# Optimization experiments

Hardware: AMD Instinct MI355X
Metric: run time of the kernel (lower is better)

The kernel has to match this reference:

```python
import jax, jax.numpy as jnp
import numpy as np

B, H, W = 4, 256, 256
DIM = 180
NH = 6
WH, WW = 16, 16          # window size
BH, BW = 8, 8            # base window size
CH = DIM // (2 * NH)     # per-head dim = 15
SCALE = float(CH)        # note: divide by head_dim (not sqrt), as in source
RH, RW = WH // BH, WW // BW
R = RH * RW              # spatial reduction ratio = 4
L = WH * WW              # 256 tokens per window
BL = BH * BW             # 64 base tokens
POS_DIM = (DIM // 4) // 4  # 11


def _rel_index(Hs, Ws):
    coords = np.stack(np.meshgrid(np.arange(Hs), np.arange(Ws), indexing='ij')).reshape(2, -1)
    rel = (coords[:, :, None] - coords[:, None, :]).transpose(1, 2, 0)
    rel[..., 0] += Hs - 1
    rel[..., 1] += Ws - 1
    rel[..., 0] *= 2 * Ws - 1
    return rel.sum(-1)  # (L, L) int

RPI = _rel_index(WH, WW)


def _ln(x, g, b):
    mu = x.mean(-1, keepdims=True)
    var = ((x - mu) ** 2).mean(-1, keepdims=True)
    return (x - mu) / jnp.sqrt(var + 1e-5) * g + b


def _conv(x, w, b):  # x: NHWC, w: HWIO
    y = jax.lax.conv_general_dilated(x, w, (1, 1), 'SAME',
                                     dimension_numbers=('NHWC', 'HWIO', 'NHWC'))
    return y + b


def setup_inputs():
    key = jax.random.key(0)
    ks = jax.random.split(key, 12)
    def wgt(k, shape, s=0.05):
        return jax.random.normal(k, shape, jnp.float32) * s
    C5 = DIM // 5
    d = {}
    d['x'] = jax.random.normal(ks[0], (B, H, W, DIM), jnp.float32)
    d['dfe_c1_w'] = wgt(ks[1], (1, 1, DIM, C5)); d['dfe_c1_b'] = jnp.zeros((C5,), jnp.float32)
    d['dfe_c2_w'] = wgt(ks[2], (3, 3, C5, C5));  d['dfe_c2_b'] = jnp.zeros((C5,), jnp.float32)
    d['dfe_c3_w'] = wgt(ks[3], (1, 1, C5, DIM)); d['dfe_c3_b'] = jnp.zeros((DIM,), jnp.float32)
    d['dfe_lin_w'] = wgt(ks[4], (1, 1, DIM, DIM)); d['dfe_lin_b'] = jnp.zeros((DIM,), jnp.float32)
    d['sl_w'] = wgt(ks[5], (1, R), 0.5); d['sl_b'] = jnp.zeros((1,), jnp.float32)
    d['pos_proj_w'] = wgt(ks[6], (POS_DIM, 2), 0.1); d['pos_proj_b'] = jnp.zeros((POS_DIM,), jnp.float32)
    for i, kk in zip((1, 2), (ks[7], ks[8])):
        d['pos%d_ln_g' % i] = jnp.ones((POS_DIM,), jnp.float32)
        d['pos%d_ln_b' % i] = jnp.zeros((POS_DIM,), jnp.float32)
        d['pos%d_w' % i] = wgt(kk, (POS_DIM, POS_DIM), 0.1)
        d['pos%d_b' % i] = jnp.zeros((POS_DIM,), jnp.float32)
    d['pos3_ln_g'] = jnp.ones((POS_DIM,), jnp.float32)
    d['pos3_ln_b'] = jnp.zeros((POS_DIM,), jnp.float32)
    d['pos3_w'] = wgt(ks[9], (NH, POS_DIM), 0.1)
    d['pos3_b'] = jnp.zeros((NH,), jnp.float32)
    d['proj_w'] = wgt(ks[10], (DIM, DIM))
    d['proj_b'] = jnp.zeros((DIM,), jnp.float32)
    return d


def reference(x, dfe_c1_w, dfe_c1_b, dfe_c2_w, dfe_c2_b, dfe_c3_w, dfe_c3_b,
              dfe_lin_w, dfe_lin_b, sl_w, sl_b, pos_proj_w, pos_proj_b,
              pos1_ln_g, pos1_ln_b, pos1_w, pos1_b,
              pos2_ln_g, pos2_ln_b, pos2_w, pos2_b,
              pos3_ln_g, pos3_ln_b, pos3_w, pos3_b,
              proj_w, proj_b):
    Bb, Hh, Ww_, C = x.shape
    # ---- DFE: qv = conv_path(x) * linear_path(x) ----
    t = jax.nn.leaky_relu(_conv(x, dfe_c1_w, dfe_c1_b), 0.2)
    t = jax.nn.leaky_relu(_conv(t, dfe_c2_w, dfe_c2_b), 0.2)
    t = _conv(t, dfe_c3_w, dfe_c3_b)
    qv = t * _conv(x, dfe_lin_w, dfe_lin_b)  # (B,H,W,C)
    # ---- window partition ----
    qv = qv.reshape(Bb, Hh // WH, WH, Ww_ // WW, WW, C).transpose(0, 1, 3, 2, 4, 5)
    qv = qv.reshape(-1, L, C)                       # (B_, L, C)
    B_ = qv.shape[0]
    qv = qv.reshape(B_, L, 2, NH, CH)
    q = qv[:, :, 0].transpose(0, 2, 1, 3)           # (B_, NH, L, CH)
    v = qv[:, :, 1].transpose(0, 2, 1, 3)           # (B_, NH, L, CH)
    # ---- spatial linear projection of v to base window ----
    vp = v.reshape(B_, NH, BH, RH, BW, RW, CH).transpose(0, 1, 2, 4, 6, 3, 5)
    vp = vp.reshape(B_, NH, BL, CH, R)
    vp = jnp.einsum('bnlcr,r->bnlc', vp, sl_w[0]) + sl_b[0]  # (B_, NH, BL, CH)
    # ---- spatial self-correlation ----
    corr = jnp.einsum('bnlc,bnmc->bnlm', q, vp) / SCALE       # (B_, NH, L, BL)
    # dynamic relative position bias (non-residual MLP)
    ph = jnp.arange(1 - WH, WH)
    pw = jnp.arange(1 - WW, WW)
    biases = jnp.stack(jnp.meshgrid(ph, pw, indexing='ij')).reshape(2, -1).T.astype(x.dtype)
    p = biases @ pos_proj_w.T + pos_proj_b
    p = jax.nn.relu(_ln(p, pos1_ln_g, pos1_ln_b)) @ pos1_w.T + pos1_b
    p = jax.nn.relu(_ln(p, pos2_ln_g, pos2_ln_b)) @ pos2_w.T + pos2_b
    pos = jax.nn.relu(_ln(p, pos3_ln_g, pos3_ln_b)) @ pos3_w.T + pos3_b  # ((2WH-1)(2WW-1), NH)
    rpb = pos[RPI.reshape(-1)].reshape(L, L, NH).transpose(2, 0, 1)      # (NH, L, L)
    rpb = rpb.reshape(NH, L, BH, RH, BW, RW).transpose(0, 1, 2, 4, 3, 5)
    rpb = rpb.reshape(NH, L, BL, R).mean(-1)                             # (NH, L, BL)
    corr = corr + rpb[None]
    x_sp = jnp.einsum('bnlm,bnmc->bnlc', corr, vp)
    x_sp = x_sp.transpose(0, 2, 1, 3).reshape(B_, L, C // 2)
    # ---- channel self-correlation (single-head) ----
    qc = q.transpose(0, 2, 1, 3).reshape(B_, L, C // 2)
    vc = v.transpose(0, 2, 1, 3).reshape(B_, L, C // 2)
    cmap = jnp.einsum('blc,bld->bcd', qc, vc) / float(L)                 # (B_, C/2, C/2)
    x_ch = jnp.einsum('bcd,bld->blc', cmap, vc)                          # (B_, L, C/2)
    # ---- window reverse + fuse ----
    def rev(a):
        c = a.shape[-1]
        a = a.reshape(Bb, Hh // WH, Ww_ // WW, WH, WW, c).transpose(0, 1, 3, 2, 4, 5)
        return a.reshape(Bb, Hh, Ww_, c)
    x_sp = rev(x_sp.reshape(B_, WH, WW, C // 2))
    x_ch = rev(x_ch.reshape(B_, WH, WW, C // 2))
    out = jnp.concatenate([x_sp, x_ch], -1) @ proj_w.T + proj_b          # (B,H,W,C)
    return out
```

## Files before the change

kernel.cpp:

```cpp
#include <hip/hip_runtime.h>

#define LEAKY(v) ((v) > 0.f ? (v) : 0.2f * (v))

__device__ __forceinline__ void ln_relu11(float* p, const float* __restrict__ g,
                                          const float* __restrict__ b) {
  float mu = 0.f;
#pragma unroll
  for (int j = 0; j < 11; ++j) mu += p[j];
  mu *= (1.f / 11.f);
  float var = 0.f;
#pragma unroll
  for (int j = 0; j < 11; ++j) { float d = p[j] - mu; var += d * d; }
  var *= (1.f / 11.f);
  float inv = 1.f / sqrtf(var + 1e-5f);
#pragma unroll
  for (int j = 0; j < 11; ++j) {
    float v = (p[j] - mu) * inv * g[j] + b[j];
    p[j] = v > 0.f ? v : 0.f;
  }
}

__global__ void pos_mlp_kernel(
    const float* __restrict__ w0, const float* __restrict__ b0,
    const float* __restrict__ g1, const float* __restrict__ be1,
    const float* __restrict__ w1, const float* __restrict__ b1,
    const float* __restrict__ g2, const float* __restrict__ be2,
    const float* __restrict__ w2, const float* __restrict__ b2,
    const float* __restrict__ g3, const float* __restrict__ be3,
    const float* __restrict__ w3, const float* __restrict__ b3,
    float* __restrict__ pos_out) {
  int r = blockIdx.x * 256 + threadIdx.x;
  if (r >= 961) return;
  float bh = (float)(r / 31 - 15);
  float bw = (float)(r % 31 - 15);
  float p[11], q[11];
#pragma unroll
  for (int j = 0; j < 11; ++j) p[j] = bh * w0[2 * j] + bw * w0[2 * j + 1] + b0[j];
  ln_relu11(p, g1, be1);
#pragma unroll
  for (int j = 0; j < 11; ++j) {
    float s = b1[j];
#pragma unroll
    for (int k = 0; k < 11; ++k) s += p[k] * w1[j * 11 + k];
    q[j] = s;
  }
  ln_relu11(q, g2, be2);
#pragma unroll
  for (int j = 0; j < 11; ++j) {
    float s = b2[j];
#pragma unroll
    for (int k = 0; k < 11; ++k) s += q[k] * w2[j * 11 + k];
    p[j] = s;
  }
  ln_relu11(p, g3, be3);
#pragma unroll
  for (int n = 0; n < 6; ++n) {
    float s = b3[n];
#pragma unroll
    for (int k = 0; k < 11; ++k) s += p[k] * w3[n * 11 + k];
    pos_out[r * 6 + n] = s;
  }
}

__global__ void rpb_kernel(const float* __restrict__ pos, float* __restrict__ rpb) {
  int o = blockIdx.x * 256 + threadIdx.x;
  int n = o >> 14;
  int l = (o >> 6) & 255;
  int m = o & 63;
  int i1 = l >> 4, j1 = l & 15;
  int bi = m >> 3, bj = m & 7;
  float s = 0.f;
#pragma unroll
  for (int rh = 0; rh < 2; ++rh)
#pragma unroll
    for (int rw = 0; rw < 2; ++rw) {
      int i2 = bi * 2 + rh, j2 = bj * 2 + rw;
      int idx = (i1 - i2 + 15) * 31 + (j1 - j2 + 15);
      s += pos[idx * 6 + n];
    }
  rpb[o] = s * 0.25f;
}

__global__ void pt_kernel(const float* __restrict__ pjw, float* __restrict__ pt) {
  int i = blockIdx.x * 256 + threadIdx.x;
  if (i >= 180 * 180) return;
  int c = i / 180, k = i % 180;
  pt[c * 180 + k] = pjw[k * 180 + c];
}

__global__ __launch_bounds__(256) void dfe1_kernel(const float* __restrict__ x,
                                                   const float* __restrict__ w1,
                                                   const float* __restrict__ b1,
                                                   float* __restrict__ t1) {
  __shared__ float xt[256][36];
  int t = threadIdx.x;
  int p0 = blockIdx.x * 256;
  float acc[36];
#pragma unroll
  for (int j = 0; j < 36; ++j) acc[j] = 0.f;
  for (int kc = 0; kc < 5; ++kc) {
    __syncthreads();
    for (int idx = t; idx < 256 * 36; idx += 256) {
      int px = idx / 36, ci = idx % 36;
      xt[px][ci] = x[(p0 + px) * 180 + kc * 36 + ci];
    }
    __syncthreads();
    for (int ci = 0; ci < 36; ++ci) {
      float v = xt[t][ci];
      const float* wr = &w1[(kc * 36 + ci) * 36];
#pragma unroll
      for (int j = 0; j < 36; ++j) acc[j] += v * wr[j];
    }
  }
  float* o = &t1[(p0 + t) * 36];
#pragma unroll
  for (int j = 0; j < 36; ++j) {
    float v = acc[j] + b1[j];
    o[j] = LEAKY(v);
  }
}

__global__ __launch_bounds__(256) void dfe2_kernel(const float* __restrict__ t1,
                                                   const float* __restrict__ w2,
                                                   const float* __restrict__ b2,
                                                   float* __restrict__ t2) {
  __shared__ float halo[18][18][36];
  int t = threadIdx.x;
  int blk = blockIdx.x;
  int img = blk >> 8;
  int rem = blk & 255;
  int ty0 = (rem >> 4) << 4;
  int tx0 = (rem & 15) << 4;
  for (int idx = t; idx < 18 * 18 * 36; idx += 256) {
    int ci = idx % 36;
    int xx = (idx / 36) % 18;
    int yy = idx / (36 * 18);
    int gy = ty0 + yy - 1;
    int gx = tx0 + xx - 1;
    float v = 0.f;
    if (gy >= 0 && gy < 256 && gx >= 0 && gx < 256)
      v = t1[((img * 256 + gy) * 256 + gx) * 36 + ci];
    halo[yy][xx][ci] = v;
  }
  __syncthreads();
  int ly = t >> 4, lx = t & 15;
  float acc[36];
#pragma unroll
  for (int j = 0; j < 36; ++j) acc[j] = 0.f;
#pragma unroll
  for (int kh = 0; kh < 3; ++kh)
#pragma unroll
    for (int kw = 0; kw < 3; ++kw) {
      for (int ci = 0; ci < 36; ++ci) {
        float v = halo[ly + kh][lx + kw][ci];
        const float* wr = &w2[((kh * 3 + kw) * 36 + ci) * 36];
#pragma unroll
        for (int j = 0; j < 36; ++j) acc[j] += v * wr[j];
      }
    }
  float* o = &t2[((img * 256 + ty0 + ly) * 256 + tx0 + lx) * 36];
#pragma unroll
  for (int j = 0; j < 36; ++j) {
    float v = acc[j] + b2[j];
    o[j] = LEAKY(v);
  }
}

__global__ __launch_bounds__(256, 2) void dfe3_kernel(const float* __restrict__ x,
                                                      const float* __restrict__ t2,
                                                      const float* __restrict__ w3,
                                                      const float* __restrict__ b3,
                                                      const float* __restrict__ wl,
                                                      const float* __restrict__ bl,
                                                      float* __restrict__ qv) {
  __shared__ __align__(16) float As[36 * 132];
  __shared__ __align__(16) float Bs[36 * 180 + 16];
  int t = threadIdx.x;
  int tx = t & 15;
  int ty = t >> 4;
  int p0 = blockIdx.x * 128;

  int pA0 = t / 9,           cA0 = t - pA0 * 9;
  int pA1 = (t + 256) / 9,   cA1 = (t + 256) - pA1 * 9;
  int pA2 = (t + 512) / 9,   cA2 = (t + 512) - pA2 * 9;
  int pA3 = (t + 768) / 9,   cA3 = (t + 768) - pA3 * 9;
  int pA4 = (t + 1024) / 9,  cA4 = (t + 1024) - pA4 * 9;
  const float4* xf4  = (const float4*)x;
  const float4* t2f4 = (const float4*)t2;
  const float4* wlf4 = (const float4*)wl;
  const float4* w3f4 = (const float4*)w3;
  float4* Bs4 = (float4*)Bs;

  float4 a0, a1, a2, a3, a4;
  float4 bF0, bF1, bF2, bF3, bF4, bF5, bF6;
  a4 = make_float4(0.f, 0.f, 0.f, 0.f);
  bF6 = make_float4(0.f, 0.f, 0.f, 0.f);

  auto scatterA = [&](int pa, int ca, float4 v) {
    As[(ca * 4 + 0) * 132 + pa] = v.x;
    As[(ca * 4 + 1) * 132 + pa] = v.y;
    As[(ca * 4 + 2) * 132 + pa] = v.z;
    As[(ca * 4 + 3) * 132 + pa] = v.w;
  };
  auto stage_write = [&]() {
    scatterA(pA0, cA0, a0);
    scatterA(pA1, cA1, a1);
    scatterA(pA2, cA2, a2);
    scatterA(pA3, cA3, a3);
    if (t < 128) scatterA(pA4, cA4, a4);
    Bs4[t] = bF0;
    Bs4[t + 256] = bF1;
    Bs4[t + 512] = bF2;
    Bs4[t + 768] = bF3;
    Bs4[t + 1024] = bF4;
    Bs4[t + 1280] = bF5;
    if (t < 84) Bs4[t + 1536] = bF6;
  };

  auto issue_lin = [&](int kc) {
    int kb = kc * 9;
    a0 = xf4[(size_t)(p0 + pA0) * 45 + kb + cA0];
    a1 = xf4[(size_t)(p0 + pA1) * 45 + kb + cA1];
    a2 = xf4[(size_t)(p0 + pA2) * 45 + kb + cA2];
    a3 = xf4[(size_t)(p0 + pA3) * 45 + kb + cA3];
    if (t < 128) a4 = xf4[(size_t)(p0 + pA4) * 45 + kb + cA4];
    int kw = kc * 1620;
    bF0 = wlf4[kw + t];
    bF1 = wlf4[kw + t + 256];
    bF2 = wlf4[kw + t + 512];
    bF3 = wlf4[kw + t + 768];
    bF4 = wlf4[kw + t + 1024];
    bF5 = wlf4[kw + t + 1280];
    if (t < 84) bF6 = wlf4[kw + t + 1536];
  };
  auto issue_conv = [&]() {
    a0 = t2f4[(size_t)(p0 + pA0) * 9 + cA0];
    a1 = t2f4[(size_t)(p0 + pA1) * 9 + cA1];
    a2 = t2f4[(size_t)(p0 + pA2) * 9 + cA2];
    a3 = t2f4[(size_t)(p0 + pA3) * 9 + cA3];
    if (t < 128) a4 = t2f4[(size_t)(p0 + pA4) * 9 + cA4];
    bF0 = w3f4[t];
    bF1 = w3f4[t + 256];
    bF2 = w3f4[t + 512];
    bF3 = w3f4[t + 768];
    bF4 = w3f4[t + 1024];
    bF5 = w3f4[t + 1280];
    if (t < 84) bF6 = w3f4[t + 1536];
  };

  auto compute36 = [&](float acc[8][12]) {
    for (int ci = 0; ci < 36; ++ci) {
      const float4* ap = (const float4*)&As[ci * 132 + ty * 8];
      float4 A0 = ap[0], A1 = ap[1];
      const float* bp = &Bs[ci * 180 + tx * 12];
      float4 B0 = *(const float4*)bp;
      float4 B1 = *(const float4*)(bp + 4);
      float4 B2 = *(const float4*)(bp + 8);
      float av[8] = {A0.x, A0.y, A0.z, A0.w, A1.x, A1.y, A1.z, A1.w};
      float bv[12] = {B0.x, B0.y, B0.z, B0.w, B1.x, B1.y, B1.z, B1.w,
                      B2.x, B2.y, B2.z, B2.w};
#pragma unroll
      for (int r = 0; r < 8; ++r)
#pragma unroll
        for (int j = 0; j < 12; ++j) acc[r][j] += av[r] * bv[j];
    }
  };

  issue_lin(0);
  float accL[8][12];
#pragma unroll
  for (int r = 0; r < 8; ++r)
#pragma unroll
    for (int j = 0; j < 12; ++j) accL[r][j] = 0.f;

#pragma unroll 1
  for (int p = 0; p < 5; ++p) {
    stage_write();
    __syncthreads();
    if (p < 4) issue_lin(p + 1); else issue_conv();
    compute36(accL);
    __syncthreads();
  }

  if (tx < 15) {
#pragma unroll
    for (int r = 0; r < 8; ++r) {
      int base = (p0 + ty * 8 + r) * 180 + tx * 12;
#pragma unroll
      for (int j = 0; j < 12; ++j) qv[base + j] = accL[r][j] + bl[tx * 12 + j];
    }
  }

  float accC[8][12];
#pragma unroll
  for (int r = 0; r < 8; ++r)
#pragma unroll
    for (int j = 0; j < 12; ++j) accC[r][j] = 0.f;
  stage_write();
  __syncthreads();
  compute36(accC);

  if (tx < 15) {
#pragma unroll
    for (int r = 0; r < 8; ++r) {
      int base = (p0 + ty * 8 + r) * 180 + tx * 12;
#pragma unroll
      for (int j = 0; j < 12; ++j) {
        float lp = qv[base + j];
        qv[base + j] = (accC[r][j] + b3[tx * 12 + j]) * lp;
      }
    }
  }
}

__global__ __launch_bounds__(256, 2) void att_sp_kernel(
    const float* __restrict__ qv, const float* __restrict__ slw,
    const float* __restrict__ slb, const float* __restrict__ rpb,
    const float* __restrict__ pt, const float* __restrict__ pb,
    float* __restrict__ out) {
  __shared__ __align__(16) float vp[6][64][16];
  __shared__ float xsp[128][91];
  int t = threadIdx.x;
  int wb = blockIdx.x;
  int b = wb >> 8, wi = (wb >> 4) & 15, wj = wb & 15;
  int wbase = (b * 256 + wi * 16) * 256 + wj * 16;
  float wsl0 = slw[0], wsl1 = slw[1], wsl2 = slw[2], wsl3 = slw[3];
  float bsl = slb[0];

  for (int idx = t; idx < 6 * 64 * 16; idx += 256) {
    int n = idx >> 10;
    int m = (idx >> 4) & 63;
    int ch = idx & 15;
    float s = 0.f;
    if (ch < 15) {
      int bi = m >> 3, bj = m & 7;
      int pa00 = (wbase + (bi * 2) * 256 + bj * 2) * 180 + 90 + n * 15 + ch;
      s = qv[pa00] * wsl0;
      s += qv[pa00 + 180] * wsl1;
      s += qv[pa00 + 256 * 180] * wsl2;
      s += qv[pa00 + 257 * 180] * wsl3;
      s += bsl;
    }
    vp[n][m][ch] = s;
  }
  __syncthreads();

  const float inv15 = 1.f / 15.f;
  int h0 = t >> 7;
  int rem = t & 127;
  int half = rem >> 6;
  int pr = rem & 63;
  int l0 = half * 128 + pr * 2;
  int l1 = l0 + 1;
  int pa0 = (wbase + (l0 >> 4) * 256 + (l0 & 15)) * 180;
  int pa1 = (wbase + (l1 >> 4) * 256 + (l1 & 15)) * 180;

  auto attn_unit = [&](int n, float (&xs0)[15], float (&xs1)[15]) {
    float qh0[15], qh1[15];
#pragma unroll
    for (int c = 0; c < 15; ++c) {
      qh0[c] = qv[pa0 + n * 15 + c];
      qh1[c] = qv[pa1 + n * 15 + c];
    }
#pragma unroll
    for (int c = 0; c < 15; ++c) { xs0[c] = 0.f; xs1[c] = 0.f; }
    const float* rpA = &rpb[(n * 256 + l0) * 64];
    const float* rpB = &rpb[(n * 256 + l1) * 64];
#pragma unroll 2
    for (int m4 = 0; m4 < 16; ++m4) {
      float4 ra = *(const float4*)(rpA + m4 * 4);
      float4 rb = *(const float4*)(rpB + m4 * 4);
      float raa[4] = {ra.x, ra.y, ra.z, ra.w};
      float rba[4] = {rb.x, rb.y, rb.z, rb.w};
#pragma unroll
      for (int mm = 0; mm < 4; ++mm) {
        const float4* vr = (const float4*)(&vp[n][m4 * 4 + mm][0]);
        float4 v0 = vr[0], v1 = vr[1], v2 = vr[2], v3 = vr[3];
        float s0 = qh0[0] * v0.x + qh0[1] * v0.y + qh0[2] * v0.z + qh0[3] * v0.w +
                   qh0[4] * v1.x + qh0[5] * v1.y + qh0[6] * v1.z + qh0[7] * v1.w +
                   qh0[8] * v2.x + qh0[9] * v2.y + qh0[10] * v2.z + qh0[11] * v2.w +
                   qh0[12] * v3.x + qh0[13] * v3.y + qh0[14] * v3.z;
        float s1 = qh1[0] * v0.x + qh1[1] * v0.y + qh1[2] * v0.z + qh1[3] * v0.w +
                   qh1[4] * v1.x + qh1[5] * v1.y + qh1[6] * v1.z + qh1[7] * v1.w +
                   qh1[8] * v2.x + qh1[9] * v2.y + qh1[10] * v2.z + qh1[11] * v2.w +
                   qh1[12] * v3.x + qh1[13] * v3.y + qh1[14] * v3.z;
        s0 = s0 * inv15 + raa[mm];
        s1 = s1 * inv15 + rba[mm];
        xs0[0] += s0 * v0.x; xs0[1] += s0 * v0.y; xs0[2] += s0 * v0.z; xs0[3] += s0 * v0.w;
        xs0[4] += s0 * v1.x; xs0[5] += s0 * v1.y; xs0[6] += s0 * v1.z; xs0[7] += s0 * v1.w;
        xs0[8] += s0 * v2.x; xs0[9] += s0 * v2.y; xs0[10] += s0 * v2.z; xs0[11] += s0 * v2.w;
        xs0[12] += s0 * v3.x; xs0[13] += s0 * v3.y; xs0[14] += s0 * v3.z;
        xs1[0] += s1 * v0.x; xs1[1] += s1 * v0.y; xs1[2] += s1 * v0.z; xs1[3] += s1 * v0.w;
        xs1[4] += s1 * v1.x; xs1[5] += s1 * v1.y; xs1[6] += s1 * v1.z; xs1[7] += s1 * v1.w;
        xs1[8] += s1 * v2.x; xs1[9] += s1 * v2.y; xs1[10] += s1 * v2.z; xs1[11] += s1 * v2.w;
        xs1[12] += s1 * v3.x; xs1[13] += s1 * v3.y; xs1[14] += s1 * v3.z;
      }
    }
  };

  float xsA0[15], xsA1[15], xsB0[15], xsB1[15], xsC0[15], xsC1[15];
  attn_unit(h0, xsA0, xsA1);
  attn_unit(h0 + 2, xsB0, xsB1);
  attn_unit(h0 + 4, xsC0, xsC1);

#pragma unroll 1
  for (int hs = 0; hs < 2; ++hs) {
    if (half == hs) {
      int r0 = pr * 2, r1 = r0 + 1;
#pragma unroll
      for (int c = 0; c < 15; ++c) {
        xsp[r0][h0 * 15 + c] = xsA0[c];
        xsp[r1][h0 * 15 + c] = xsA1[c];
        xsp[r0][(h0 + 2) * 15 + c] = xsB0[c];
        xsp[r1][(h0 + 2) * 15 + c] = xsB1[c];
        xsp[r0][(h0 + 4) * 15 + c] = xsC0[c];
        xsp[r1][(h0 + 4) * 15 + c] = xsC1[c];
      }
    }
    __syncthreads();
    {
      int lane = t & 63;
      int w4 = __builtin_amdgcn_readfirstlane(t >> 6);
      int k0 = w4 * 45;
      const float* ptb = pt + k0;
#pragma unroll 1
      for (int tok2 = 0; tok2 < 2; ++tok2) {
        int tt = tok2 * 64 + lane;
        int l2 = hs * 128 + tt;
        int pa2 = (wbase + (l2 >> 4) * 256 + (l2 & 15)) * 180 + k0;
        float pacc[45];
#pragma unroll
        for (int j = 0; j < 45; ++j) pacc[j] = pb[k0 + j];
#pragma unroll 2
        for (int c = 0; c < 90; ++c) {
          float xv = xsp[tt][c];
          const float* prw = ptb + c * 180;
#pragma unroll
          for (int j = 0; j < 45; ++j) pacc[j] += xv * prw[j];
        }
        float* op = out + pa2;
#pragma unroll
        for (int j = 0; j < 45; ++j) op[j] = pacc[j];
      }
    }
    __syncthreads();
  }
}

__global__ __launch_bounds__(256, 2) void cmapM_kernel(const float* __restrict__ qv,
                                                       const float* __restrict__ p2t,
                                                       float* __restrict__ M) {
  __shared__ float cmt[90][91];
  __shared__ float bufA[32][97];
  __shared__ float vtt[32][97];
  int t = threadIdx.x;
  int wb = blockIdx.x;
  int b = wb >> 8, wi = (wb >> 4) & 15, wj = wb & 15;
  int wbase = (b * 256 + wi * 16) * 256 + wj * 16;

  int tx = t & 15, ty = t >> 4;
  float acc[6][6];
#pragma unroll
  for (int i = 0; i < 6; ++i)
#pragma unroll
    for (int j = 0; j < 6; ++j) acc[i][j] = 0.f;

#pragma unroll 1
  for (int ck = 0; ck < 8; ++ck) {
    __syncthreads();
    for (int idx = t; idx < 32 * 97; idx += 256) {
      int l = idx / 97, c = idx % 97;
      int gl = ck * 32 + l;
      int pa = (wbase + (gl >> 4) * 256 + (gl & 15)) * 180;
      bufA[l][c] = (c < 90) ? qv[pa + c] : 0.f;
      vtt[l][c] = (c < 90) ? qv[pa + 90 + c] : 0.f;
    }
    __syncthreads();
    for (int lk = 0; lk < 32; ++lk) {
      float aa[6], bb[6];
#pragma unroll
      for (int i = 0; i < 6; ++i) aa[i] = bufA[lk][tx * 6 + i];
#pragma unroll
      for (int j = 0; j < 6; ++j) bb[j] = vtt[lk][ty * 6 + j];
#pragma unroll
      for (int i = 0; i < 6; ++i)
#pragma unroll
        for (int j = 0; j < 6; ++j) acc[i][j] += aa[i] * bb[j];
    }
  }
  __syncthreads();
  if (tx < 15 && ty < 15) {
#pragma unroll
    for (int i = 0; i < 6; ++i)
#pragma unroll
      for (int j = 0; j < 6; ++j) cmt[tx * 6 + i][ty * 6 + j] = acc[i][j] * (1.f / 256.f);
  }
  __syncthreads();

  int lane = t & 63;
  int kq = __builtin_amdgcn_readfirstlane(t >> 6);
  int k0 = kq * 45;
  int d0 = lane;
  int d1 = lane + 64;
  int d1c = (d1 < 90) ? d1 : 0;
  float m0[45], m1[45];
#pragma unroll
  for (int j = 0; j < 45; ++j) { m0[j] = 0.f; m1[j] = 0.f; }
#pragma unroll 1
  for (int c = 0; c < 90; ++c) {
    const float* pr = p2t + c * 180 + k0;
    float v0 = cmt[c][d0];
    float v1 = cmt[c][d1c];
#pragma unroll
    for (int j = 0; j < 45; ++j) {
      float p = pr[j];
      m0[j] += p * v0;
      m1[j] += p * v1;
    }
  }
  float* M0 = M + (size_t)wb * 16200 + d0 * 180 + k0;
#pragma unroll
  for (int j = 0; j < 45; ++j) M0[j] = m0[j];
  if (d1 < 90) {
    float* M1 = M + (size_t)wb * 16200 + d1 * 180 + k0;
#pragma unroll
    for (int j = 0; j < 45; ++j) M1[j] = m1[j];
  }
}

__global__ __launch_bounds__(256, 4) void chupd_kernel(const float* __restrict__ qv,
                                                       const float* __restrict__ M,
                                                       float* __restrict__ out) {
  __shared__ float vt[64][91];
  int bid = blockIdx.x;
  int wb = bid >> 2, grp = bid & 3;
  int b = wb >> 8, wi = (wb >> 4) & 15, wj = wb & 15;
  int wbase = (b * 256 + wi * 16) * 256 + wj * 16;
  int t = threadIdx.x;

  for (int idx = t; idx < 64 * 90; idx += 256) {
    int l = idx / 90, d = idx - l * 90;
    int gl = grp * 64 + l;
    int pa = (wbase + (gl >> 4) * 256 + (gl & 15)) * 180;
    vt[l][d] = qv[pa + 90 + d];
  }
  __syncthreads();

  int l = t & 63;
  int kq = __builtin_amdgcn_readfirstlane(t >> 6);
  int k0 = kq * 45;
  const float* Mw = M + (size_t)wb * 16200;
  float pacc[45];
#pragma unroll
  for (int j = 0; j < 45; ++j) pacc[j] = 0.f;
#pragma unroll 2
  for (int d = 0; d < 90; ++d) {
    const float* mr = Mw + d * 180 + k0;
    float vl = vt[l][d];
#pragma unroll
    for (int j = 0; j < 45; ++j) pacc[j] += mr[j] * vl;
  }
  int gl = grp * 64 + l;
  int pa = (wbase + (gl >> 4) * 256 + (gl & 15)) * 180 + k0;
#pragma unroll
  for (int j = 0; j < 45; ++j) out[pa + j] += pacc[j];
}

extern "C" void kernel_launch(void* const* d_in, const int* in_sizes, int n_in,
                              void* d_out, int out_size, void* d_ws, size_t ws_size,
                              hipStream_t stream) {
  (void)in_sizes; (void)n_in; (void)out_size; (void)ws_size;
  const float* x   = (const float*)d_in[0];
  const float* w1  = (const float*)d_in[1];
  const float* b1  = (const float*)d_in[2];
  const float* w2  = (const float*)d_in[3];
  const float* b2  = (const float*)d_in[4];
  const float* w3  = (const float*)d_in[5];
  const float* b3  = (const float*)d_in[6];
  const float* wl  = (const float*)d_in[7];
  const float* bl  = (const float*)d_in[8];
  const float* slw = (const float*)d_in[9];
  const float* slb = (const float*)d_in[10];
  const float* pw0 = (const float*)d_in[11];
  const float* pb0 = (const float*)d_in[12];
  const float* g1  = (const float*)d_in[13];
  const float* be1 = (const float*)d_in[14];
  const float* mw1 = (const float*)d_in[15];
  const float* mb1 = (const float*)d_in[16];
  const float* g2  = (const float*)d_in[17];
  const float* be2 = (const float*)d_in[18];
  const float* mw2 = (const float*)d_in[19];
  const float* mb2 = (const float*)d_in[20];
  const float* g3  = (const float*)d_in[21];
  const float* be3 = (const float*)d_in[22];
  const float* mw3 = (const float*)d_in[23];
  const float* mb3 = (const float*)d_in[24];
  const float* pjw = (const float*)d_in[25];
  const float* pjb = (const float*)d_in[26];
  float* out = (float*)d_out;
  float* ws  = (float*)d_ws;

  float* qv  = ws;
  float* t1  = ws + 47185920;
  float* t2  = t1 + 9437184;
  float* pos = t2 + 9437184;
  float* rpb = pos + 5768;
  float* M   = t1;
  float* pt  = t1 + 18874368 - 32768;

  pos_mlp_kernel<<<4, 256, 0, stream>>>(pw0, pb0, g1, be1, mw1, mb1,
                                        g2, be2, mw2, mb2, g3, be3, mw3, mb3, pos);
  rpb_kernel<<<384, 256, 0, stream>>>(pos, rpb);
  dfe1_kernel<<<1024, 256, 0, stream>>>(x, w1, b1, t1);
  dfe2_kernel<<<1024, 256, 0, stream>>>(t1, w2, b2, t2);
  dfe3_kernel<<<2048, 256, 0, stream>>>(x, t2, w3, b3, wl, bl, qv);
  pt_kernel<<<127, 256, 0, stream>>>(pjw, pt);
  att_sp_kernel<<<1024, 256, 0, stream>>>(qv, slw, slb, rpb, pt, pjb, out);
  cmapM_kernel<<<1024, 256, 0, stream>>>(qv, pt + 90 * 180, M);
  chupd_kernel<<<4096, 256, 0, stream>>>(qv, M, out);
}
```

Baseline: 1.419 ms.

## Restructure spatial attention to one token per thread for higher occupancy

```diff
diff --git a/kernel.cpp b/kernel.cpp
--- a/kernel.cpp
+++ b/kernel.cpp
@@ -313,7 +313,7 @@
   }
 }
 
-__global__ __launch_bounds__(256, 2) void att_sp_kernel(
+__global__ __launch_bounds__(256, 4) void att_sp_kernel(
     const float* __restrict__ qv, const float* __restrict__ slw,
     const float* __restrict__ slb, const float* __restrict__ rpb,
     const float* __restrict__ pt, const float* __restrict__ pb,
@@ -345,77 +345,51 @@
   }
   __syncthreads();
 
+  int lt = t & 127;
+  int hg = t >> 7;
   const float inv15 = 1.f / 15.f;
-  int h0 = t >> 7;
-  int rem = t & 127;
-  int half = rem >> 6;
-  int pr = rem & 63;
-  int l0 = half * 128 + pr * 2;
-  int l1 = l0 + 1;
-  int pa0 = (wbase + (l0 >> 4) * 256 + (l0 & 15)) * 180;
-  int pa1 = (wbase + (l1 >> 4) * 256 + (l1 & 15)) * 180;
-
-  auto attn_unit = [&](int n, float (&xs0)[15], float (&xs1)[15]) {
-    float qh0[15], qh1[15];
-#pragma unroll
-    for (int c = 0; c < 15; ++c) {
-      qh0[c] = qv[pa0 + n * 15 + c];
-      qh1[c] = qv[pa1 + n * 15 + c];
-    }
-#pragma unroll
-    for (int c = 0; c < 15; ++c) { xs0[c] = 0.f; xs1[c] = 0.f; }
-    const float* rpA = &rpb[(n * 256 + l0) * 64];
-    const float* rpB = &rpb[(n * 256 + l1) * 64];
-#pragma unroll 2
-    for (int m4 = 0; m4 < 16; ++m4) {
-      float4 ra = *(const float4*)(rpA + m4 * 4);
-      float4 rb = *(const float4*)(rpB + m4 * 4);
-      float raa[4] = {ra.x, ra.y, ra.z, ra.w};
-      float rba[4] = {rb.x, rb.y, rb.z, rb.w};
-#pragma unroll
-      for (int mm = 0; mm < 4; ++mm) {
-        const float4* vr = (const float4*)(&vp[n][m4 * 4 + mm][0]);
-        float4 v0 = vr[0], v1 = vr[1], v2 = vr[2], v3 = vr[3];
-        float s0 = qh0[0] * v0.x + qh0[1] * v0.y + qh0[2] * v0.z + qh0[3] * v0.w +
-                   qh0[4] * v1.x + qh0[5] * v1.y + qh0[6] * v1.z + qh0[7] * v1.w +
-                   qh0[8] * v2.x + qh0[9] * v2.y + qh0[10] * v2.z + qh0[11] * v2.w +
-                   qh0[12] * v3.x + qh0[13] * v3.y + qh0[14] * v3.z;
-        float s1 = qh1[0] * v0.x + qh1[1] * v0.y + qh1[2] * v0.z + qh1[3] * v0.w +
-                   qh1[4] * v1.x + qh1[5] * v1.y + qh1[6] * v1.z + qh1[7] * v1.w +
-                   qh1[8] * v2.x + qh1[9] * v2.y + qh1[10] * v2.z + qh1[11] * v2.w +
-                   qh1[12] * v3.x + qh1[13] * v3.y + qh1[14] * v3.z;
-        s0 = s0 * inv15 + raa[mm];
-        s1 = s1 * inv15 + rba[mm];
-        xs0[0] += s0 * v0.x; xs0[1] += s0 * v0.y; xs0[2] += s0 * v0.z; xs0[3] += s0 * v0.w;
-        xs0[4] += s0 * v1.x; xs0[5] += s0 * v1.y; xs0[6] += s0 * v1.z; xs0[7] += s0 * v1.w;
-        xs0[8] += s0 * v2.x; xs0[9] += s0 * v2.y; xs0[10] += s0 * v2.z; xs0[11] += s0 * v2.w;
-        xs0[12] += s0 * v3.x; xs0[13] += s0 * v3.y; xs0[14] += s0 * v3.z;
-        xs1[0] += s1 * v0.x; xs1[1] += s1 * v0.y; xs1[2] += s1 * v0.z; xs1[3] += s1 * v0.w;
-        xs1[4] += s1 * v1.x; xs1[5] += s1 * v1.y; xs1[6] += s1 * v1.z; xs1[7] += s1 * v1.w;
-        xs1[8] += s1 * v2.x; xs1[9] += s1 * v2.y; xs1[10] += s1 * v2.z; xs1[11] += s1 * v2.w;
-        xs1[12] += s1 * v3.x; xs1[13] += s1 * v3.y; xs1[14] += s1 * v3.z;
+
+#pragma unroll 1
+  for (int half = 0; half < 2; ++half) {
+    int l = half * 128 + lt;
+    int pa = (wbase + (l >> 4) * 256 + (l & 15)) * 180;
+#pragma unroll 1
+    for (int nn = 0; nn < 3; ++nn) {
+      int n = hg * 3 + nn;
+      float qh[15];
+#pragma unroll
+      for (int c = 0; c < 15; ++c) qh[c] = qv[pa + n * 15 + c];
+      float xs[15];
+#pragma unroll
+      for (int c = 0; c < 15; ++c) xs[c] = 0.f;
+      const float* rp = &rpb[(n * 256 + l) * 64];
+#pragma unroll 4
+      for (int m4 = 0; m4 < 16; ++m4) {
+        float4 rpv = *(const float4*)(rp + m4 * 4);
+        float rparr[4] = {rpv.x, rpv.y, rpv.z, rpv.w};
+#pragma unroll
+        for (int mm = 0; mm < 4; ++mm) {
+          const float4* vr = (const float4*)(&vp[n][m4 * 4 + mm][0]);
+          float4 v0 = vr[0], v1 = vr[1], v2 = vr[2], v3 = vr[3];
+          float d0 = qh[0] * v0.x + qh[1] * v0.y;
+          float d1 = qh[2] * v0.z + qh[3] * v0.w;
+          float d2 = qh[4] * v1.x + qh[5] * v1.y;
+          float d3 = qh[6] * v1.z + qh[7] * v1.w;
+          float d4 = qh[8] * v2.x + qh[9] * v2.y;
+          float d5 = qh[10] * v2.z + qh[11] * v2.w;
+          float d6 = qh[12] * v3.x + qh[13] * v3.y;
+          float d7 = qh[14] * v3.z;
+          float e0 = d0 + d1, e1 = d2 + d3, e2 = d4 + d5, e3 = d6 + d7;
+          float s = (e0 + e1) + (e2 + e3);
+          s = s * inv15 + rparr[mm];
+          xs[0] += s * v0.x; xs[1] += s * v0.y; xs[2] += s * v0.z; xs[3] += s * v0.w;
+          xs[4] += s * v1.x; xs[5] += s * v1.y; xs[6] += s * v1.z; xs[7] += s * v1.w;
+          xs[8] += s * v2.x; xs[9] += s * v2.y; xs[10] += s * v2.z; xs[11] += s * v2.w;
+          xs[12] += s * v3.x; xs[13] += s * v3.y; xs[14] += s * v3.z;
+        }
       }
-    }
-  };
-
-  float xsA0[15], xsA1[15], xsB0[15], xsB1[15], xsC0[15], xsC1[15];
-  attn_unit(h0, xsA0, xsA1);
-  attn_unit(h0 + 2, xsB0, xsB1);
-  attn_unit(h0 + 4, xsC0, xsC1);
-
-#pragma unroll 1
-  for (int hs = 0; hs < 2; ++hs) {
-    if (half == hs) {
-      int r0 = pr * 2, r1 = r0 + 1;
-#pragma unroll
-      for (int c = 0; c < 15; ++c) {
-        xsp[r0][h0 * 15 + c] = xsA0[c];
-        xsp[r1][h0 * 15 + c] = xsA1[c];
-        xsp[r0][(h0 + 2) * 15 + c] = xsB0[c];
-        xsp[r1][(h0 + 2) * 15 + c] = xsB1[c];
-        xsp[r0][(h0 + 4) * 15 + c] = xsC0[c];
-        xsp[r1][(h0 + 4) * 15 + c] = xsC1[c];
-      }
+#pragma unroll
+      for (int c = 0; c < 15; ++c) xsp[lt][n * 15 + c] = xs[c];
     }
     __syncthreads();
     {
@@ -426,7 +400,7 @@
 #pragma unroll 1
       for (int tok2 = 0; tok2 < 2; ++tok2) {
         int tt = tok2 * 64 + lane;
-        int l2 = hs * 128 + tt;
+        int l2 = half * 128 + tt;
         int pa2 = (wbase + (l2 >> 4) * 256 + (l2 & 15)) * 180 + k0;
         float pacc[45];
 #pragma unroll
```

Measured after the change: 1.346 ms. 5.1% less time.
